# Optimization experiments

Hardware: AMD Instinct MI355X
Metric: run time of the kernel (lower is better)

## Reference

```python
import jax, jax.numpy as jnp
import numpy as np

B, L, D, H = 4, 2048, 1024, 64  # batch, seq, d_model, head_size

def setup_inputs() -> dict:
    key = jax.random.key(0)
    k1, k2 = jax.random.split(key)
    x = jax.random.normal(k1, (B, L, D), dtype=jnp.float32)
    # nn.Linear(d_model, head_size, bias=False) weight: [head_size, d_model]
    Wq = jax.random.normal(k2, (H, D), dtype=jnp.float32) * (1.0 / np.sqrt(D))
    return {"x": x, "Wq": Wq}

def reference(x, Wq):
    # Faithful to source bug: q, k, v ALL use the query projection.
    q = jnp.einsum('bld,hd->blh', x, Wq)
    k = q
    v = q
    d_k = x.shape[-1]  # source uses d_model, not head_size
    scores = jnp.einsum('blh,bmh->blm', q, k) / jnp.sqrt(jnp.float32(d_k))
    Lq = x.shape[1]
    causal = jnp.tril(jnp.ones((Lq, Lq), dtype=bool))
    scores = jnp.where(causal, scores, -jnp.inf)
    attn = jax.nn.softmax(scores, axis=-1)
    # dropout in eval mode -> identity
    return jnp.einsum('blm,bmh->blh', attn, v)
```

## Files before the change

### kernel.cpp

```cpp
#include <hip/hip_runtime.h>
#include <hip/hip_bf16.h>
#include <cmath>

#define Bb 4
#define Ll 2048
#define Dd 1024
#define Hh 64

typedef float f32x4 __attribute__((ext_vector_type(4)));
typedef short s16x8 __attribute__((ext_vector_type(8)));

#if __has_builtin(__builtin_amdgcn_exp2f)
#define EXP2(x) __builtin_amdgcn_exp2f(x)
#else
#define EXP2(x) exp2f(x)
#endif
#define SCL 0.0450842200278f

__device__ __forceinline__ unsigned int pk2(float a, float b) {
    float2 f; f.x = a; f.y = b;
    union { __hip_bfloat162 h; unsigned int u; } c;
    c.h = __float22bfloat162_rn(f);
    return c.u;
}
__device__ __forceinline__ unsigned short f2bf(float f) {
    union { float f; unsigned int u; } v; v.f = f;
    unsigned int u = v.u;
    return (unsigned short)((u + 0x7FFFu + ((u >> 16) & 1u)) >> 16);
}

__global__ __launch_bounds__(256) void proj_mfma(const float* __restrict__ x,
                                                 const float* __restrict__ Wq,
                                                 unsigned short* __restrict__ q,
                                                 unsigned short* __restrict__ qT) {
    __shared__ float red[4 * 64 * 20];
    const int t = threadIdx.x;
    const int lane = t & 63;
    const int wv = t >> 6;
    const int m15 = lane & 15, q_ = lane >> 4;
    const int row0 = blockIdx.x * 16;
    const float* xr = x + (size_t)(row0 + m15) * Dd + wv * 256 + q_ * 8;
    const float* wr0 = Wq + (size_t)m15 * Dd + wv * 256 + q_ * 8;

    f32x4 acc[4];
#pragma unroll
    for (int i = 0; i < 4; ++i) acc[i] = (f32x4){0.f, 0.f, 0.f, 0.f};

#pragma unroll
    for (int ks = 0; ks < 8; ++ks) {
        float4 a = *(const float4*)(xr + ks * 32);
        float4 b = *(const float4*)(xr + ks * 32 + 4);
        union { s16x8 v; uint4 u; } A;
        A.u.x = pk2(a.x, a.y); A.u.y = pk2(a.z, a.w);
        A.u.z = pk2(b.x, b.y); A.u.w = pk2(b.z, b.w);
#pragma unroll
        for (int ct = 0; ct < 4; ++ct) {
            const float* wr = wr0 + (size_t)ct * 16 * Dd + ks * 32;
            float4 wa = *(const float4*)wr;
            float4 wb = *(const float4*)(wr + 4);
            union { s16x8 v; uint4 u; } B;
            B.u.x = pk2(wa.x, wa.y); B.u.y = pk2(wa.z, wa.w);
            B.u.z = pk2(wb.x, wb.y); B.u.w = pk2(wb.z, wb.w);
            acc[ct] = __builtin_amdgcn_mfma_f32_16x16x32_bf16(A.v, B.v, acc[ct], 0, 0, 0);
        }
    }
#pragma unroll
    for (int ct = 0; ct < 4; ++ct)
        *(f32x4*)&red[(wv * 64 + ct * 16 + m15) * 20 + q_ * 4] = acc[ct];
    __syncthreads();
    const int col = t >> 2, r4 = (t & 3) * 4;
    f32x4 sum = *(const f32x4*)&red[(0 * 64 + col) * 20 + r4];
#pragma unroll
    for (int v = 1; v < 4; ++v) sum += *(const f32x4*)&red[(v * 64 + col) * 20 + r4];
    unsigned short u0 = f2bf(sum[0]), u1 = f2bf(sum[1]), u2 = f2bf(sum[2]), u3 = f2bf(sum[3]);
    q[(size_t)(row0 + r4 + 0) * Hh + col] = u0;
    q[(size_t)(row0 + r4 + 1) * Hh + col] = u1;
    q[(size_t)(row0 + r4 + 2) * Hh + col] = u2;
    q[(size_t)(row0 + r4 + 3) * Hh + col] = u3;
    ushort4 pk; pk.x = u0; pk.y = u1; pk.z = u2; pk.w = u3;
    const int b = row0 >> 11;
    *(ushort4*)&qT[((size_t)(b * Hh + col)) * Ll + (row0 & 2047) + r4] = pk;
}

__global__ __launch_bounds__(256, 3) void flash_mfma(const unsigned short* __restrict__ qg,
                                                     const unsigned short* __restrict__ qTg,
                                                     float* __restrict__ PO,
                                                     float* __restrict__ ML,
                                                     float* __restrict__ out) {
    const int i = blockIdx.x;
    const int b = blockIdx.y;
    int g = (int)((sqrtf(1.0f + 2.0f * (float)i) - 1.0f) * 0.5f);
    while (2 * g * (g + 1) > i) --g;
    while (2 * (g + 1) * (g + 2) <= i) ++g;
    const int r_ = i - 2 * g * (g + 1);
    const int qt = 4 * g + r_ / (g + 1);
    const int s  = r_ % (g + 1);
    const int ns = g + 1;

    __shared__ uint4 Qs4[512], Ks4[512], Vt4[512];
    __shared__ __align__(16) unsigned short Pb[4 * 16 * 72];
    const int t = threadIdx.x, lane = t & 63, w = t >> 6;
    const int m15 = lane & 15, q_ = lane >> 4;
    const unsigned short* qb  = qg  + (size_t)b * Ll * Hh;
    const unsigned short* qTb = qTg + (size_t)b * Hh * Ll;

#pragma unroll
    for (int j = 0; j < 2; ++j) {
        int idx = t + j * 256;
        int r = idx >> 3, hc = idx & 7;
        Qs4[hc * 64 + (r ^ hc)] = *(const uint4*)(qb + (size_t)(qt * 64 + r) * Hh + hc * 8);
    }
    f32x4 Oacc[4];
#pragma unroll
    for (int k = 0; k < 4; ++k) Oacc[k] = (f32x4){0.f, 0.f, 0.f, 0.f};
    float mr = -INFINITY, lr = 0.f;
    const int n_it = min(4, qt - 4 * s + 1);
    const int c_base = s * 256;
    const int row = qt * 64 + w * 16 + m15;
    unsigned short* Pr = Pb + (w * 16 + m15) * 72;

    for (int it = 0; it < n_it; ++it) {
        const int c0 = c_base + it * 64;
        __syncthreads();
#pragma unroll
        for (int j = 0; j < 2; ++j) {
            int idx = t + j * 256;
            int c = idx >> 3, hc = idx & 7;
            Ks4[hc * 64 + (c ^ hc)] = *(const uint4*)(qb + (size_t)(c0 + c) * Hh + hc * 8);
        }
#pragma unroll
        for (int j = 0; j < 2; ++j) {
            int idx = t + j * 256;
            int h = idx >> 3, cc = idx & 7;
            Vt4[cc * 64 + (h ^ cc)] = *(const uint4*)(qTb + (size_t)h * Ll + c0 + cc * 8);
        }
        __syncthreads();
        f32x4 sc[4];
#pragma unroll
        for (int ct = 0; ct < 4; ++ct) sc[ct] = (f32x4){0.f, 0.f, 0.f, 0.f};
#pragma unroll
        for (int ks = 0; ks < 2; ++ks) {
            int hc = ks * 4 + q_;
            s16x8 Bq = *(const s16x8*)&Qs4[hc * 64 + ((w * 16 + m15) ^ hc)];
#pragma unroll
            for (int ct = 0; ct < 4; ++ct) {
                s16x8 Ak = *(const s16x8*)&Ks4[hc * 64 + ((ct * 16 + m15) ^ hc)];
                sc[ct] = __builtin_amdgcn_mfma_f32_16x16x32_bf16(Ak, Bq, sc[ct], 0, 0, 0);
            }
        }
        const bool diag = (4 * s + it) == qt;
        float v[16];
#pragma unroll
        for (int ct = 0; ct < 4; ++ct)
#pragma unroll
            for (int r = 0; r < 4; ++r) {
                float sv = sc[ct][r] * SCL;
                if (diag && (c0 + ct * 16 + q_ * 4 + r > row)) sv = -INFINITY;
                v[ct * 4 + r] = sv;
            }
        float vmax = v[0];
#pragma unroll
        for (int k = 1; k < 16; ++k) vmax = fmaxf(vmax, v[k]);
        vmax = fmaxf(vmax, __shfl_xor(vmax, 16, 64));
        vmax = fmaxf(vmax, __shfl_xor(vmax, 32, 64));
        float mnew = fmaxf(mr, vmax);
        float alpha = EXP2(mr - mnew);
        float p[16];
        float psum = 0.f;
#pragma unroll
        for (int k = 0; k < 16; ++k) { p[k] = EXP2(v[k] - mnew); psum += p[k]; }
        psum += __shfl_xor(psum, 16, 64);
        psum += __shfl_xor(psum, 32, 64);
        lr = lr * alpha + psum;
        mr = mnew;
#pragma unroll
        for (int ht = 0; ht < 4; ++ht) Oacc[ht] *= alpha;
#pragma unroll
        for (int ct = 0; ct < 4; ++ct) {
            uint2 pr; pr.x = pk2(p[ct * 4 + 0], p[ct * 4 + 1]);
            pr.y = pk2(p[ct * 4 + 2], p[ct * 4 + 3]);
            *(uint2*)(Pr + ct * 16 + q_ * 4) = pr;
        }
#pragma unroll
        for (int kc = 0; kc < 2; ++kc) {
            int cc = kc * 4 + q_;
            s16x8 Bp = *(const s16x8*)(Pr + kc * 32 + q_ * 8);
#pragma unroll
            for (int ht = 0; ht < 4; ++ht) {
                s16x8 Av = *(const s16x8*)&Vt4[cc * 64 + ((ht * 16 + m15) ^ cc)];
                Oacc[ht] = __builtin_amdgcn_mfma_f32_16x16x32_bf16(Av, Bp, Oacc[ht], 0, 0, 0);
            }
        }
    }

    if (ns == 1) {
        const float inv = 1.0f / lr;
#pragma unroll
        for (int ht = 0; ht < 4; ++ht)
            *(f32x4*)&out[(size_t)(b * Ll + qt * 64 + w * 16 + m15) * 64 + ht * 16 + q_ * 4]
                = Oacc[ht] * inv;
        return;
    }
    const int bq = b * 32 + qt;
    const size_t base = ((size_t)(bq * 8 + s)) * 4096;
#pragma unroll
    for (int ht = 0; ht < 4; ++ht)
        *(f32x4*)&PO[base + (size_t)(w * 16 + m15) * 64 + ht * 16 + q_ * 4] = Oacc[ht];
    if (q_ == 0) {
        float* mlp = ML + ((size_t)(bq * 8 + s)) * 128;
        mlp[(w * 16 + m15) * 2 + 0] = mr;
        mlp[(w * 16 + m15) * 2 + 1] = lr;
    }
}

__global__ __launch_bounds__(256) void combine_k(const float* __restrict__ PO,
                                                 const float* __restrict__ ML,
                                                 float* __restrict__ out) {
    const int b = blockIdx.x / 28;
    const int qt = blockIdx.x % 28 + 4;
    const int bq = b * 32 + qt;
    const int ns = (qt >> 2) + 1;
    const int t = threadIdx.x;
    const int r = blockIdx.y * 32 + (t >> 3);
    const int c8 = (t & 7) * 8;
    const float* mlp = ML + (size_t)bq * 8 * 128;
    const float* pob = PO + (size_t)bq * 8 * 4096;
    float M = -INFINITY;
    for (int si = 0; si < ns; ++si) M = fmaxf(M, mlp[si * 128 + r * 2]);
    float L = 0.f;
    f32x4 a0 = {0.f, 0.f, 0.f, 0.f}, a1 = a0;
    for (int si = 0; si < ns; ++si) {
        float ms = mlp[si * 128 + r * 2], ls = mlp[si * 128 + r * 2 + 1];
        float wgt = EXP2(ms - M);
        L += ls * wgt;
        const f32x4* sp = (const f32x4*)(pob + (size_t)si * 4096 + r * 64 + c8);
        a0 += wgt * sp[0];
        a1 += wgt * sp[1];
    }
    float inv = 1.0f / L;
    f32x4* op = (f32x4*)(out + (size_t)(b * Ll + qt * 64 + r) * 64 + c8);
    op[0] = a0 * inv;
    op[1] = a1 * inv;
}

extern "C" void kernel_launch(void* const* d_in, const int* in_sizes, int n_in,
                              void* d_out, int out_size, void* d_ws, size_t ws_size,
                              hipStream_t stream) {
    const float* x  = (const float*)d_in[0];
    const float* Wq = (const float*)d_in[1];
    float* out = (float*)d_out;
    char* ws = (char*)d_ws;
    unsigned short* q  = (unsigned short*)ws;
    unsigned short* qT = (unsigned short*)(ws + (1 << 20));
    float* PO = (float*)(ws + (2 << 20));
    float* ML = (float*)(ws + (18 << 20));

    proj_mfma<<<512, 256, 0, stream>>>(x, Wq, q, qT);
    flash_mfma<<<dim3(144, Bb), 256, 0, stream>>>(q, qT, PO, ML, out);
    combine_k<<<dim3(112, 2), 256, 0, stream>>>(PO, ML, out);
}
```

Before: 105.8 us.

## Fuse projection, flash attention and combine into one cooperative persistent kernel

Replaces the three kernel launches with a single cooperative kernel that runs projection, split-KV flash attention and the combine step as grid-stride phases separated by grid-wide syncs. The goal is to remove launch gaps and per-kernel tail effects. Partial outputs are now stored as bf16 instead of fp32, which halves that intermediate traffic but costs some precision in the combine. Grid syncs add their own overhead, and the grid size depends on the occupancy query; the old three-kernel path is kept as a fallback if the cooperative launch fails.

Result: slower. 172.6 us (+63.1%).

```diff
diff --git a/kernel.cpp b/kernel.cpp
--- a/kernel.cpp
+++ b/kernel.cpp
@@ -1,6 +1,9 @@
 #include <hip/hip_runtime.h>
 #include <hip/hip_bf16.h>
+#include <hip/hip_cooperative_groups.h>
 #include <cmath>
+
+namespace cg = cooperative_groups;
 
 #define Bb 4
 #define Ll 2048
@@ -27,6 +30,243 @@
     union { float f; unsigned int u; } v; v.f = f;
     unsigned int u = v.u;
     return (unsigned short)((u + 0x7FFFu + ((u >> 16) & 1u)) >> 16);
+}
+__device__ __forceinline__ float blo(unsigned int u) {
+    union { float f; unsigned int x; } v; v.x = u << 16; return v.f;
+}
+__device__ __forceinline__ float bhi(unsigned int u) {
+    union { float f; unsigned int x; } v; v.x = u & 0xffff0000u; return v.f;
+}
+
+__global__ __launch_bounds__(256, 2) void fused_all(const float* __restrict__ x,
+                                                    const float* __restrict__ Wq,
+                                                    unsigned short* __restrict__ q,
+                                                    unsigned short* __restrict__ qT,
+                                                    unsigned short* __restrict__ PO,
+                                                    float* __restrict__ ML,
+                                                    float* __restrict__ out) {
+    cg::grid_group grid = cg::this_grid();
+    __shared__ union {
+        struct { float red[4 * 64 * 20]; } p;
+        struct { uint4 Qs4[512]; uint4 Ks4[512]; uint4 Vt4[512];
+                 unsigned short Pb[4 * 16 * 72]; } f;
+    } sm;
+    const int G = gridDim.x;
+    const int bid = blockIdx.x;
+    const int t = threadIdx.x, lane = t & 63, w = t >> 6;
+    const int m15 = lane & 15, q_ = lane >> 4;
+
+    for (int rb = bid; rb < 512; rb += G) {
+        const int row0 = rb * 16;
+        const float* xr = x + (size_t)(row0 + m15) * Dd + w * 256 + q_ * 8;
+        const float* wr0 = Wq + (size_t)m15 * Dd + w * 256 + q_ * 8;
+        f32x4 acc[4];
+#pragma unroll
+        for (int i = 0; i < 4; ++i) acc[i] = (f32x4){0.f, 0.f, 0.f, 0.f};
+#pragma unroll
+        for (int ks = 0; ks < 8; ++ks) {
+            float4 a = *(const float4*)(xr + ks * 32);
+            float4 b = *(const float4*)(xr + ks * 32 + 4);
+            union { s16x8 v; uint4 u; } A;
+            A.u.x = pk2(a.x, a.y); A.u.y = pk2(a.z, a.w);
+            A.u.z = pk2(b.x, b.y); A.u.w = pk2(b.z, b.w);
+#pragma unroll
+            for (int ct = 0; ct < 4; ++ct) {
+                const float* wr = wr0 + (size_t)ct * 16 * Dd + ks * 32;
+                float4 wa = *(const float4*)wr;
+                float4 wb = *(const float4*)(wr + 4);
+                union { s16x8 v; uint4 u; } B;
+                B.u.x = pk2(wa.x, wa.y); B.u.y = pk2(wa.z, wa.w);
+                B.u.z = pk2(wb.x, wb.y); B.u.w = pk2(wb.z, wb.w);
+                acc[ct] = __builtin_amdgcn_mfma_f32_16x16x32_bf16(A.v, B.v, acc[ct], 0, 0, 0);
+            }
+        }
+#pragma unroll
+        for (int ct = 0; ct < 4; ++ct)
+            *(f32x4*)&sm.p.red[(w * 64 + ct * 16 + m15) * 20 + q_ * 4] = acc[ct];
+        __syncthreads();
+        const int col = t >> 2, r4 = (t & 3) * 4;
+        f32x4 sum = *(const f32x4*)&sm.p.red[(0 * 64 + col) * 20 + r4];
+#pragma unroll
+        for (int v = 1; v < 4; ++v) sum += *(const f32x4*)&sm.p.red[(v * 64 + col) * 20 + r4];
+        unsigned short u0 = f2bf(sum[0]), u1 = f2bf(sum[1]), u2 = f2bf(sum[2]), u3 = f2bf(sum[3]);
+        q[(size_t)(row0 + r4 + 0) * Hh + col] = u0;
+        q[(size_t)(row0 + r4 + 1) * Hh + col] = u1;
+        q[(size_t)(row0 + r4 + 2) * Hh + col] = u2;
+        q[(size_t)(row0 + r4 + 3) * Hh + col] = u3;
+        ushort4 pkv; pkv.x = u0; pkv.y = u1; pkv.z = u2; pkv.w = u3;
+        const int bb = row0 >> 11;
+        *(ushort4*)&qT[((size_t)(bb * Hh + col)) * Ll + (row0 & 2047) + r4] = pkv;
+        __syncthreads();
+    }
+
+    grid.sync();
+
+    for (int u = bid; u < 576; u += G) {
+        const int b = u / 144;
+        const int i = u % 144;
+        int g = (int)((sqrtf(1.0f + 2.0f * (float)i) - 1.0f) * 0.5f);
+        while (2 * g * (g + 1) > i) --g;
+        while (2 * (g + 1) * (g + 2) <= i) ++g;
+        const int r_ = i - 2 * g * (g + 1);
+        const int qt = 4 * g + r_ / (g + 1);
+        const int s  = r_ % (g + 1);
+        const int ns = g + 1;
+        const unsigned short* qb  = q  + (size_t)b * Ll * Hh;
+        const unsigned short* qTb = qT + (size_t)b * Hh * Ll;
+
+        __syncthreads();
+#pragma unroll
+        for (int j = 0; j < 2; ++j) {
+            int idx = t + j * 256;
+            int r = idx >> 3, hc = idx & 7;
+            sm.f.Qs4[hc * 64 + (r ^ hc)] =
+                *(const uint4*)(qb + (size_t)(qt * 64 + r) * Hh + hc * 8);
+        }
+        f32x4 Oacc[4];
+#pragma unroll
+        for (int k = 0; k < 4; ++k) Oacc[k] = (f32x4){0.f, 0.f, 0.f, 0.f};
+        float mr = -INFINITY, lr = 0.f;
+        const int n_it = min(4, qt - 4 * s + 1);
+        const int c_base = s * 256;
+        const int row = qt * 64 + w * 16 + m15;
+        unsigned short* Pr = sm.f.Pb + (w * 16 + m15) * 72;
+
+        for (int it = 0; it < n_it; ++it) {
+            const int c0 = c_base + it * 64;
+            __syncthreads();
+#pragma unroll
+            for (int j = 0; j < 2; ++j) {
+                int idx = t + j * 256;
+                int c = idx >> 3, hc = idx & 7;
+                sm.f.Ks4[hc * 64 + (c ^ hc)] =
+                    *(const uint4*)(qb + (size_t)(c0 + c) * Hh + hc * 8);
+            }
+#pragma unroll
+            for (int j = 0; j < 2; ++j) {
+                int idx = t + j * 256;
+                int h = idx >> 3, cc = idx & 7;
+                sm.f.Vt4[cc * 64 + (h ^ cc)] =
+                    *(const uint4*)(qTb + (size_t)h * Ll + c0 + cc * 8);
+            }
+            __syncthreads();
+            f32x4 sc[4];
+#pragma unroll
+            for (int ct = 0; ct < 4; ++ct) sc[ct] = (f32x4){0.f, 0.f, 0.f, 0.f};
+#pragma unroll
+            for (int ks = 0; ks < 2; ++ks) {
+                int hc = ks * 4 + q_;
+                s16x8 Bq = *(const s16x8*)&sm.f.Qs4[hc * 64 + ((w * 16 + m15) ^ hc)];
+#pragma unroll
+                for (int ct = 0; ct < 4; ++ct) {
+                    s16x8 Ak = *(const s16x8*)&sm.f.Ks4[hc * 64 + ((ct * 16 + m15) ^ hc)];
+                    sc[ct] = __builtin_amdgcn_mfma_f32_16x16x32_bf16(Ak, Bq, sc[ct], 0, 0, 0);
+                }
+            }
+            const bool diag = (4 * s + it) == qt;
+            float v[16];
+#pragma unroll
+            for (int ct = 0; ct < 4; ++ct)
+#pragma unroll
+                for (int r = 0; r < 4; ++r) {
+                    float sv = sc[ct][r] * SCL;
+                    if (diag && (c0 + ct * 16 + q_ * 4 + r > row)) sv = -INFINITY;
+                    v[ct * 4 + r] = sv;
+                }
+            float vmax = v[0];
+#pragma unroll
+            for (int k = 1; k < 16; ++k) vmax = fmaxf(vmax, v[k]);
+            vmax = fmaxf(vmax, __shfl_xor(vmax, 16, 64));
+            vmax = fmaxf(vmax, __shfl_xor(vmax, 32, 64));
+            float mnew = fmaxf(mr, vmax);
+            float alpha = EXP2(mr - mnew);
+            float p[16];
+            float psum = 0.f;
+#pragma unroll
+            for (int k = 0; k < 16; ++k) { p[k] = EXP2(v[k] - mnew); psum += p[k]; }
+            psum += __shfl_xor(psum, 16, 64);
+            psum += __shfl_xor(psum, 32, 64);
+            lr = lr * alpha + psum;
+            mr = mnew;
+#pragma unroll
+            for (int ht = 0; ht < 4; ++ht) Oacc[ht] *= alpha;
+#pragma unroll
+            for (int ct = 0; ct < 4; ++ct) {
+                uint2 pr; pr.x = pk2(p[ct * 4 + 0], p[ct * 4 + 1]);
+                pr.y = pk2(p[ct * 4 + 2], p[ct * 4 + 3]);
+                *(uint2*)(Pr + ct * 16 + q_ * 4) = pr;
+            }
+#pragma unroll
+            for (int kc = 0; kc < 2; ++kc) {
+                int cc = kc * 4 + q_;
+                s16x8 Bp = *(const s16x8*)(Pr + kc * 32 + q_ * 8);
+#pragma unroll
+                for (int ht = 0; ht < 4; ++ht) {
+                    s16x8 Av = *(const s16x8*)&sm.f.Vt4[cc * 64 + ((ht * 16 + m15) ^ cc)];
+                    Oacc[ht] = __builtin_amdgcn_mfma_f32_16x16x32_bf16(Av, Bp, Oacc[ht], 0, 0, 0);
+                }
+            }
+        }
+        if (ns == 1) {
+            const float inv = 1.0f / lr;
+#pragma unroll
+            for (int ht = 0; ht < 4; ++ht)
+                *(f32x4*)&out[(size_t)(b * Ll + qt * 64 + w * 16 + m15) * 64 + ht * 16 + q_ * 4]
+                    = Oacc[ht] * inv;
+        } else {
+            const int bq = b * 32 + qt;
+            const size_t base = ((size_t)(bq * 8 + s)) * 4096;
+#pragma unroll
+            for (int ht = 0; ht < 4; ++ht) {
+                ushort4 pw;
+                pw.x = f2bf(Oacc[ht][0]); pw.y = f2bf(Oacc[ht][1]);
+                pw.z = f2bf(Oacc[ht][2]); pw.w = f2bf(Oacc[ht][3]);
+                *(ushort4*)&PO[base + (size_t)(w * 16 + m15) * 64 + ht * 16 + q_ * 4] = pw;
+            }
+            if (q_ == 0) {
+                float* mlp = ML + ((size_t)(bq * 8 + s)) * 128;
+                mlp[(w * 16 + m15) * 2 + 0] = mr;
+                mlp[(w * 16 + m15) * 2 + 1] = lr;
+            }
+        }
+    }
+
+    grid.sync();
+
+    for (int cb = bid; cb < 224; cb += G) {
+        const int b = cb / 56;
+        const int rem = cb % 56;
+        const int qt = 4 + rem / 2;
+        const int half = rem & 1;
+        const int bq = b * 32 + qt;
+        const int ns = (qt >> 2) + 1;
+        const int r = half * 32 + (t >> 3);
+        const int c8 = (t & 7) * 8;
+        const float* mlp = ML + (size_t)bq * 1024;
+        const unsigned short* pob = PO + (size_t)bq * 32768;
+        float M = -INFINITY;
+        for (int si = 0; si < ns; ++si) M = fmaxf(M, mlp[si * 128 + r * 2]);
+        float L = 0.f;
+        float a[8];
+#pragma unroll
+        for (int k = 0; k < 8; ++k) a[k] = 0.f;
+        for (int si = 0; si < ns; ++si) {
+            float ms = mlp[si * 128 + r * 2], ls = mlp[si * 128 + r * 2 + 1];
+            float wgt = EXP2(ms - M);
+            L += ls * wgt;
+            uint4 pv = *(const uint4*)(pob + (size_t)si * 4096 + r * 64 + c8);
+            a[0] += wgt * blo(pv.x); a[1] += wgt * bhi(pv.x);
+            a[2] += wgt * blo(pv.y); a[3] += wgt * bhi(pv.y);
+            a[4] += wgt * blo(pv.z); a[5] += wgt * bhi(pv.z);
+            a[6] += wgt * blo(pv.w); a[7] += wgt * bhi(pv.w);
+        }
+        const float inv = 1.0f / L;
+        float* op = out + (size_t)(b * Ll + qt * 64 + r) * 64 + c8;
+        f32x4 o0 = {a[0] * inv, a[1] * inv, a[2] * inv, a[3] * inv};
+        f32x4 o1 = {a[4] * inv, a[5] * inv, a[6] * inv, a[7] * inv};
+        *(f32x4*)op = o0;
+        *(f32x4*)(op + 4) = o1;
+    }
 }
 
 __global__ __launch_bounds__(256) void proj_mfma(const float* __restrict__ x,
@@ -41,11 +281,9 @@
     const int row0 = blockIdx.x * 16;
     const float* xr = x + (size_t)(row0 + m15) * Dd + wv * 256 + q_ * 8;
     const float* wr0 = Wq + (size_t)m15 * Dd + wv * 256 + q_ * 8;
-
     f32x4 acc[4];
 #pragma unroll
     for (int i = 0; i < 4; ++i) acc[i] = (f32x4){0.f, 0.f, 0.f, 0.f};
-
 #pragma unroll
     for (int ks = 0; ks < 8; ++ks) {
         float4 a = *(const float4*)(xr + ks * 32);
@@ -77,9 +315,9 @@
     q[(size_t)(row0 + r4 + 1) * Hh + col] = u1;
     q[(size_t)(row0 + r4 + 2) * Hh + col] = u2;
     q[(size_t)(row0 + r4 + 3) * Hh + col] = u3;
-    ushort4 pk; pk.x = u0; pk.y = u1; pk.z = u2; pk.w = u3;
+    ushort4 pkv; pkv.x = u0; pkv.y = u1; pkv.z = u2; pkv.w = u3;
     const int b = row0 >> 11;
-    *(ushort4*)&qT[((size_t)(b * Hh + col)) * Ll + (row0 & 2047) + r4] = pk;
+    *(ushort4*)&qT[((size_t)(b * Hh + col)) * Ll + (row0 & 2047) + r4] = pkv;
 }
 
 __global__ __launch_bounds__(256, 3) void flash_mfma(const unsigned short* __restrict__ qg,
@@ -96,14 +334,12 @@
     const int qt = 4 * g + r_ / (g + 1);
     const int s  = r_ % (g + 1);
     const int ns = g + 1;
-
     __shared__ uint4 Qs4[512], Ks4[512], Vt4[512];
     __shared__ __align__(16) unsigned short Pb[4 * 16 * 72];
     const int t = threadIdx.x, lane = t & 63, w = t >> 6;
     const int m15 = lane & 15, q_ = lane >> 4;
     const unsigned short* qb  = qg  + (size_t)b * Ll * Hh;
     const unsigned short* qTb = qTg + (size_t)b * Hh * Ll;
-
 #pragma unroll
     for (int j = 0; j < 2; ++j) {
         int idx = t + j * 256;
@@ -118,7 +354,6 @@
     const int c_base = s * 256;
     const int row = qt * 64 + w * 16 + m15;
     unsigned short* Pr = Pb + (w * 16 + m15) * 72;
-
     for (int it = 0; it < n_it; ++it) {
         const int c0 = c_base + it * 64;
         __syncthreads();
@@ -192,7 +427,6 @@
             }
         }
     }
-
     if (ns == 1) {
         const float inv = 1.0f / lr;
 #pragma unroll
@@ -250,12 +484,31 @@
     const float* Wq = (const float*)d_in[1];
     float* out = (float*)d_out;
     char* ws = (char*)d_ws;
-    unsigned short* q  = (unsigned short*)ws;
-    unsigned short* qT = (unsigned short*)(ws + (1 << 20));
-    float* PO = (float*)(ws + (2 << 20));
-    float* ML = (float*)(ws + (18 << 20));
-
-    proj_mfma<<<512, 256, 0, stream>>>(x, Wq, q, qT);
-    flash_mfma<<<dim3(144, Bb), 256, 0, stream>>>(q, qT, PO, ML, out);
-    combine_k<<<dim3(112, 2), 256, 0, stream>>>(PO, ML, out);
-}
+    unsigned short* q   = (unsigned short*)ws;
+    unsigned short* qT  = (unsigned short*)(ws + (1 << 20));
+    unsigned short* POb = (unsigned short*)(ws + (2 << 20));
+    float* ML  = (float*)(ws + (10 << 20));
+    float* POf = (float*)(ws + (11 << 20));
+    float* MLf = (float*)(ws + (27 << 20));
+
+    int nb = 0;
+    hipError_t oe = hipOccupancyMaxActiveBlocksPerMultiprocessor(
+        &nb, (const void*)fused_all, 256, 0);
+    if (oe != hipSuccess) nb = 0;
+    int G = nb * 256;
+    if (G > 512) G = 512;
+
+    bool launched = false;
+    if (G >= 128) {
+        void* args[] = {(void*)&x, (void*)&Wq, (void*)&q, (void*)&qT,
+                        (void*)&POb, (void*)&ML, (void*)&out};
+        hipError_t e = hipLaunchCooperativeKernel((const void*)fused_all,
+                                                  dim3(G), dim3(256), args, 0, stream);
+        launched = (e == hipSuccess);
+    }
+    if (!launched) {
+        proj_mfma<<<512, 256, 0, stream>>>(x, Wq, q, qT);
+        flash_mfma<<<dim3(144, Bb), 256, 0, stream>>>(q, qT, POf, MLf, out);
+        combine_k<<<dim3(112, 2), 256, 0, stream>>>(POf, MLf, out);
+    }
+}
```

## Make each wave own an independent 16-row query tile and drop LDS staging

Applied to the files above, without the earlier changes.

The flash kernel now assigns an independent 16-row query tile and key split to each wavefront. Q is kept in registers and K/V fragments are read directly from global memory, which removes the shared-memory staging and block-wide barriers. Partial outputs are stored in bf16 instead of fp32, roughly halving split-partial traffic, and the combine kernel is remapped to the 16-row tiles. This gives finer-grained load balance across the causal triangle, but adds redundant global/L2 reads of K/V per wave and reduces the precision of the partial results.

After: 116.6 us. 1.1x slower.

```diff
diff --git a/kernel.cpp b/kernel.cpp
--- a/kernel.cpp
+++ b/kernel.cpp
@@ -27,6 +27,12 @@
     union { float f; unsigned int u; } v; v.f = f;
     unsigned int u = v.u;
     return (unsigned short)((u + 0x7FFFu + ((u >> 16) & 1u)) >> 16);
+}
+__device__ __forceinline__ float blo(unsigned int u) {
+    union { float f; unsigned int x; } v; v.x = u << 16; return v.f;
+}
+__device__ __forceinline__ float bhi(unsigned int u) {
+    union { float f; unsigned int x; } v; v.x = u & 0xffff0000u; return v.f;
 }
 
 __global__ __launch_bounds__(256) void proj_mfma(const float* __restrict__ x,
@@ -45,7 +51,6 @@
     f32x4 acc[4];
 #pragma unroll
     for (int i = 0; i < 4; ++i) acc[i] = (f32x4){0.f, 0.f, 0.f, 0.f};
-
 #pragma unroll
     for (int ks = 0; ks < 8; ++ks) {
         float4 a = *(const float4*)(xr + ks * 32);
@@ -77,78 +82,64 @@
     q[(size_t)(row0 + r4 + 1) * Hh + col] = u1;
     q[(size_t)(row0 + r4 + 2) * Hh + col] = u2;
     q[(size_t)(row0 + r4 + 3) * Hh + col] = u3;
-    ushort4 pk; pk.x = u0; pk.y = u1; pk.z = u2; pk.w = u3;
+    ushort4 pkv; pkv.x = u0; pkv.y = u1; pkv.z = u2; pkv.w = u3;
     const int b = row0 >> 11;
-    *(ushort4*)&qT[((size_t)(b * Hh + col)) * Ll + (row0 & 2047) + r4] = pk;
-}
-
-__global__ __launch_bounds__(256, 3) void flash_mfma(const unsigned short* __restrict__ qg,
+    *(ushort4*)&qT[((size_t)(b * Hh + col)) * Ll + (row0 & 2047) + r4] = pkv;
+}
+
+__global__ __launch_bounds__(256, 2) void flash_wave(const unsigned short* __restrict__ qg,
                                                      const unsigned short* __restrict__ qTg,
-                                                     float* __restrict__ PO,
+                                                     unsigned short* __restrict__ PO,
                                                      float* __restrict__ ML,
                                                      float* __restrict__ out) {
-    const int i = blockIdx.x;
-    const int b = blockIdx.y;
-    int g = (int)((sqrtf(1.0f + 2.0f * (float)i) - 1.0f) * 0.5f);
-    while (2 * g * (g + 1) > i) --g;
-    while (2 * (g + 1) * (g + 2) <= i) ++g;
-    const int r_ = i - 2 * g * (g + 1);
-    const int qt = 4 * g + r_ / (g + 1);
-    const int s  = r_ % (g + 1);
-    const int ns = g + 1;
-
-    __shared__ uint4 Qs4[512], Ks4[512], Vt4[512];
     __shared__ __align__(16) unsigned short Pb[4 * 16 * 72];
     const int t = threadIdx.x, lane = t & 63, w = t >> 6;
     const int m15 = lane & 15, q_ = lane >> 4;
+    const int u = blockIdx.x * 4 + w;
+    const int b = u / 576;
+    const int i = u % 576;
+    int g = 0, base = 0;
+    for (;;) {
+        int sz = 4 * ((g + 4) >> 2);
+        if (base + sz <= i) { base += sz; ++g; } else break;
+    }
+    const int nsg = (g + 4) >> 2;
+    const int r_ = i - base;
+    const int qt16 = 4 * g + r_ / nsg;
+    const int s = r_ % nsg;
+    const int nt = g + 1;
+    const int n_it = min(4, nt - 4 * s);
+
     const unsigned short* qb  = qg  + (size_t)b * Ll * Hh;
     const unsigned short* qTb = qTg + (size_t)b * Hh * Ll;
-
-#pragma unroll
-    for (int j = 0; j < 2; ++j) {
-        int idx = t + j * 256;
-        int r = idx >> 3, hc = idx & 7;
-        Qs4[hc * 64 + (r ^ hc)] = *(const uint4*)(qb + (size_t)(qt * 64 + r) * Hh + hc * 8);
-    }
+    const int row = qt16 * 16 + m15;
+    unsigned short* Pr = Pb + (w * 16 + m15) * 72;
+
+    s16x8 Bq0 = *(const s16x8*)(qb + (size_t)row * Hh + q_ * 8);
+    s16x8 Bq1 = *(const s16x8*)(qb + (size_t)row * Hh + 32 + q_ * 8);
+
     f32x4 Oacc[4];
 #pragma unroll
     for (int k = 0; k < 4; ++k) Oacc[k] = (f32x4){0.f, 0.f, 0.f, 0.f};
     float mr = -INFINITY, lr = 0.f;
-    const int n_it = min(4, qt - 4 * s + 1);
-    const int c_base = s * 256;
-    const int row = qt * 64 + w * 16 + m15;
-    unsigned short* Pr = Pb + (w * 16 + m15) * 72;
 
     for (int it = 0; it < n_it; ++it) {
-        const int c0 = c_base + it * 64;
-        __syncthreads();
-#pragma unroll
-        for (int j = 0; j < 2; ++j) {
-            int idx = t + j * 256;
-            int c = idx >> 3, hc = idx & 7;
-            Ks4[hc * 64 + (c ^ hc)] = *(const uint4*)(qb + (size_t)(c0 + c) * Hh + hc * 8);
-        }
-#pragma unroll
-        for (int j = 0; j < 2; ++j) {
-            int idx = t + j * 256;
-            int h = idx >> 3, cc = idx & 7;
-            Vt4[cc * 64 + (h ^ cc)] = *(const uint4*)(qTb + (size_t)h * Ll + c0 + cc * 8);
-        }
-        __syncthreads();
+        const int j = 4 * s + it;
+        const int c0 = j * 64;
+        const unsigned short* kb = qb + (size_t)(c0 + m15) * Hh + q_ * 8;
         f32x4 sc[4];
 #pragma unroll
         for (int ct = 0; ct < 4; ++ct) sc[ct] = (f32x4){0.f, 0.f, 0.f, 0.f};
 #pragma unroll
         for (int ks = 0; ks < 2; ++ks) {
-            int hc = ks * 4 + q_;
-            s16x8 Bq = *(const s16x8*)&Qs4[hc * 64 + ((w * 16 + m15) ^ hc)];
+            const s16x8 Bq = ks ? Bq1 : Bq0;
 #pragma unroll
             for (int ct = 0; ct < 4; ++ct) {
-                s16x8 Ak = *(const s16x8*)&Ks4[hc * 64 + ((ct * 16 + m15) ^ hc)];
+                s16x8 Ak = *(const s16x8*)(kb + ct * 16 * Hh + ks * 32);
                 sc[ct] = __builtin_amdgcn_mfma_f32_16x16x32_bf16(Ak, Bq, sc[ct], 0, 0, 0);
             }
         }
-        const bool diag = (4 * s + it) == qt;
+        const bool diag = (j == g);
         float v[16];
 #pragma unroll
         for (int ct = 0; ct < 4; ++ct)
@@ -181,66 +172,66 @@
             pr.y = pk2(p[ct * 4 + 2], p[ct * 4 + 3]);
             *(uint2*)(Pr + ct * 16 + q_ * 4) = pr;
         }
+        const unsigned short* vb = qTb + (size_t)m15 * Ll + c0 + q_ * 8;
 #pragma unroll
         for (int kc = 0; kc < 2; ++kc) {
-            int cc = kc * 4 + q_;
             s16x8 Bp = *(const s16x8*)(Pr + kc * 32 + q_ * 8);
 #pragma unroll
             for (int ht = 0; ht < 4; ++ht) {
-                s16x8 Av = *(const s16x8*)&Vt4[cc * 64 + ((ht * 16 + m15) ^ cc)];
+                s16x8 Av = *(const s16x8*)(vb + (size_t)ht * 16 * Ll + kc * 32);
                 Oacc[ht] = __builtin_amdgcn_mfma_f32_16x16x32_bf16(Av, Bp, Oacc[ht], 0, 0, 0);
             }
         }
     }
 
-    if (ns == 1) {
+    if (nsg == 1) {
         const float inv = 1.0f / lr;
 #pragma unroll
         for (int ht = 0; ht < 4; ++ht)
-            *(f32x4*)&out[(size_t)(b * Ll + qt * 64 + w * 16 + m15) * 64 + ht * 16 + q_ * 4]
-                = Oacc[ht] * inv;
+            *(f32x4*)&out[(size_t)(b * Ll + row) * Hh + ht * 16 + q_ * 4] = Oacc[ht] * inv;
         return;
     }
-    const int bq = b * 32 + qt;
-    const size_t base = ((size_t)(bq * 8 + s)) * 4096;
-#pragma unroll
-    for (int ht = 0; ht < 4; ++ht)
-        *(f32x4*)&PO[base + (size_t)(w * 16 + m15) * 64 + ht * 16 + q_ * 4] = Oacc[ht];
+    const size_t pbase = ((size_t)((b * 128 + qt16) * 8 + s)) * 1024;
+#pragma unroll
+    for (int ht = 0; ht < 4; ++ht) {
+        ushort4 pw;
+        pw.x = f2bf(Oacc[ht][0]); pw.y = f2bf(Oacc[ht][1]);
+        pw.z = f2bf(Oacc[ht][2]); pw.w = f2bf(Oacc[ht][3]);
+        *(ushort4*)&PO[pbase + (size_t)m15 * 64 + ht * 16 + q_ * 4] = pw;
+    }
     if (q_ == 0) {
-        float* mlp = ML + ((size_t)(bq * 8 + s)) * 128;
-        mlp[(w * 16 + m15) * 2 + 0] = mr;
-        mlp[(w * 16 + m15) * 2 + 1] = lr;
-    }
-}
-
-__global__ __launch_bounds__(256) void combine_k(const float* __restrict__ PO,
+        float* mlp = ML + ((size_t)((b * 128 + qt16) * 8 + s)) * 32;
+        mlp[m15 * 2 + 0] = mr;
+        mlp[m15 * 2 + 1] = lr;
+    }
+}
+
+__global__ __launch_bounds__(256) void combine_k(const unsigned short* __restrict__ PO,
                                                  const float* __restrict__ ML,
                                                  float* __restrict__ out) {
-    const int b = blockIdx.x / 28;
-    const int qt = blockIdx.x % 28 + 4;
-    const int bq = b * 32 + qt;
-    const int ns = (qt >> 2) + 1;
+    const int b = blockIdx.x / 112;
+    const int qt16 = 16 + blockIdx.x % 112;
+    const int ns = ((qt16 >> 2) + 4) >> 2;
     const int t = threadIdx.x;
-    const int r = blockIdx.y * 32 + (t >> 3);
-    const int c8 = (t & 7) * 8;
-    const float* mlp = ML + (size_t)bq * 8 * 128;
-    const float* pob = PO + (size_t)bq * 8 * 4096;
+    const int r = t >> 4;
+    const int c4 = (t & 15) * 4;
+    const float* mlp = ML + ((size_t)(b * 128 + qt16) * 8) * 32;
+    const unsigned short* pob = PO + ((size_t)(b * 128 + qt16) * 8) * 1024;
     float M = -INFINITY;
-    for (int si = 0; si < ns; ++si) M = fmaxf(M, mlp[si * 128 + r * 2]);
+    for (int si = 0; si < ns; ++si) M = fmaxf(M, mlp[si * 32 + r * 2]);
     float L = 0.f;
-    f32x4 a0 = {0.f, 0.f, 0.f, 0.f}, a1 = a0;
+    float a0 = 0.f, a1 = 0.f, a2 = 0.f, a3 = 0.f;
     for (int si = 0; si < ns; ++si) {
-        float ms = mlp[si * 128 + r * 2], ls = mlp[si * 128 + r * 2 + 1];
+        float ms = mlp[si * 32 + r * 2], ls = mlp[si * 32 + r * 2 + 1];
         float wgt = EXP2(ms - M);
         L += ls * wgt;
-        const f32x4* sp = (const f32x4*)(pob + (size_t)si * 4096 + r * 64 + c8);
-        a0 += wgt * sp[0];
-        a1 += wgt * sp[1];
-    }
-    float inv = 1.0f / L;
-    f32x4* op = (f32x4*)(out + (size_t)(b * Ll + qt * 64 + r) * 64 + c8);
-    op[0] = a0 * inv;
-    op[1] = a1 * inv;
+        uint2 pv = *(const uint2*)(pob + (size_t)si * 1024 + r * 64 + c4);
+        a0 += wgt * blo(pv.x); a1 += wgt * bhi(pv.x);
+        a2 += wgt * blo(pv.y); a3 += wgt * bhi(pv.y);
+    }
+    const float inv = 1.0f / L;
+    f32x4 o; o[0] = a0 * inv; o[1] = a1 * inv; o[2] = a2 * inv; o[3] = a3 * inv;
+    *(f32x4*)&out[(size_t)(b * Ll + qt16 * 16 + r) * Hh + c4] = o;
 }
 
 extern "C" void kernel_launch(void* const* d_in, const int* in_sizes, int n_in,
@@ -252,10 +243,10 @@
     char* ws = (char*)d_ws;
     unsigned short* q  = (unsigned short*)ws;
     unsigned short* qT = (unsigned short*)(ws + (1 << 20));
-    float* PO = (float*)(ws + (2 << 20));
-    float* ML = (float*)(ws + (18 << 20));
+    unsigned short* PO = (unsigned short*)(ws + (2 << 20));
+    float* ML = (float*)(ws + (10 << 20));
 
     proj_mfma<<<512, 256, 0, stream>>>(x, Wq, q, qT);
-    flash_mfma<<<dim3(144, Bb), 256, 0, stream>>>(q, qT, PO, ML, out);
-    combine_k<<<dim3(112, 2), 256, 0, stream>>>(PO, ML, out);
-}
+    flash_wave<<<576, 256, 0, stream>>>(q, qT, PO, ML, out);
+    combine_k<<<448, 256, 0, stream>>>(PO, ML, out);
+}
```
